# Performance work log

Measured on AMD Instinct MI355X. Metric: run time of the kernel, lower is better.

## Reference

```python
import jax, jax.numpy as jnp
import numpy as np

N_NODES = 100000
N_EDGES = 1600000
D_IN = 256
D_OUT = 128


def setup_inputs() -> dict:
    key = jax.random.key(0)
    k1, k2, k3, k4, k5, k6 = jax.random.split(key, 6)
    x = jax.random.normal(k1, (N_NODES, D_IN), dtype=jnp.float32)
    edge_src = jax.random.randint(k2, (N_EDGES,), 0, N_NODES, dtype=jnp.int32)
    edge_dst = jax.random.randint(k3, (N_EDGES,), 0, N_NODES, dtype=jnp.int32)
    edge_w = jax.random.uniform(k4, (N_EDGES,), dtype=jnp.float32)
    # GraphConvolution parameters (glorot-style scale)
    W = jax.random.normal(k5, (D_IN, D_OUT), dtype=jnp.float32) / np.sqrt(D_IN)
    b = jax.random.normal(k6, (D_OUT,), dtype=jnp.float32) * 0.01
    return {"x": x, "edge_src": edge_src, "edge_dst": edge_dst,
            "edge_w": edge_w, "W": W, "b": b}


def reference(x, edge_src, edge_dst, edge_w, W, b):
    # GraphConvolution: out = adj @ (x @ W) + b, adj given as weighted edge list
    support = x @ W                                   # [N, D_OUT] dense GEMM
    msgs = support[edge_src] * edge_w[:, None]        # [E, D_OUT] gather + scale
    out = jax.ops.segment_sum(msgs, edge_dst, num_segments=N_NODES)  # scatter-add
    return out + b
```

## Files before the change

kernel.cpp:

```cpp
#include <hip/hip_runtime.h>

#define N_NODES 100000
#define N_EDGES 1600000
#define D_IN 256
#define D_OUT 128

#define NPB 128
#define NB 782
#define REGION 2432
#define CHUNK 4096
#define NCHUNK 391
#define GEMM_BLOCKS 782

typedef __attribute__((ext_vector_type(8))) short bf16x8;
typedef __attribute__((ext_vector_type(4))) float f32x4;

__device__ __forceinline__ unsigned short f2bf(float f) {
    unsigned u = __float_as_uint(f);
    u += 0x7FFF + ((u >> 16) & 1);
    return (unsigned short)(u >> 16);
}
__device__ __forceinline__ float bflo(unsigned p) { return __uint_as_float(p << 16); }
__device__ __forceinline__ float bfhi(unsigned p) { return __uint_as_float(p & 0xFFFF0000u); }

__global__ void prep_kernel(const float* __restrict__ W,
                            unsigned short* __restrict__ Wt) {
    int idx = blockIdx.x * 256 + threadIdx.x;
    if (idx < D_OUT * D_IN) {
        int c = idx >> 8;
        int k = idx & 255;
        Wt[idx] = f2bf(W[(size_t)k * D_OUT + c]);
    }
}

union FusedSmem {
    int hist[NB];
    unsigned short wt[128 * 256];
};

__global__ __launch_bounds__(256) void fusedA_kernel(
        const float* __restrict__ x,
        const unsigned short* __restrict__ Wt,
        unsigned short* __restrict__ supb,
        const int* __restrict__ dst,
        int* __restrict__ counts) {
    __shared__ FusedSmem sm;
    int tid = threadIdx.x;

    if (blockIdx.x < NCHUNK) {
        int* hist = sm.hist;
        int e0 = blockIdx.x * CHUNK;
        for (int i = tid; i < NB; i += 256) hist[i] = 0;
        __syncthreads();
#pragma unroll
        for (int k = 0; k < 16; ++k) {
            int e = e0 + k * 256 + tid;
            if (e < N_EDGES) atomicAdd(&hist[dst[e] >> 7], 1);
        }
        __syncthreads();
        int* crow = counts + (size_t)blockIdx.x * NB;
        for (int i = tid; i < NB; i += 256) crow[i] = hist[i];
    } else {
        {
            const int4* wg = (const int4*)Wt;
            char* wl = (char*)sm.wt;
            for (int i = tid; i < 4096; i += 256) {
                int off = i * 16;
                int col = off >> 9;
                int soff = off ^ ((col & 7) << 4);
                *(int4*)(wl + soff) = wg[i];
            }
        }
        __syncthreads();

        int gb = blockIdx.x - NCHUNK;
        int w = tid >> 6;
        int lane = tid & 63;
        int r0 = (gb * 4 + w) * 32;
        int rowA0 = r0 + (lane & 15);
        int rowA1 = rowA0 + 16;
        int rowA0c = rowA0 < N_NODES ? rowA0 : N_NODES - 1;
        int rowA1c = rowA1 < N_NODES ? rowA1 : N_NODES - 1;
        int kgrp = (lane >> 4) * 8;

        f32x4 acc0[8], acc1[8];
#pragma unroll
        for (int t = 0; t < 8; ++t) {
            acc0[t] = (f32x4){0.f, 0.f, 0.f, 0.f};
            acc1[t] = (f32x4){0.f, 0.f, 0.f, 0.f};
        }

        const float* xr0 = x + (size_t)rowA0c * D_IN + kgrp;
        const float* xr1 = x + (size_t)rowA1c * D_IN + kgrp;
        int colbase = lane & 15;
        const char* wl = (const char*)sm.wt;

#pragma unroll
        for (int ks = 0; ks < 8; ++ks) {
            int k0 = ks * 32;
            float4 a0 = *(const float4*)(xr0 + k0);
            float4 a1 = *(const float4*)(xr0 + k0 + 4);
            float4 c0 = *(const float4*)(xr1 + k0);
            float4 c1 = *(const float4*)(xr1 + k0 + 4);
            bf16x8 af0, af1;
            af0[0] = (short)f2bf(a0.x); af0[1] = (short)f2bf(a0.y);
            af0[2] = (short)f2bf(a0.z); af0[3] = (short)f2bf(a0.w);
            af0[4] = (short)f2bf(a1.x); af0[5] = (short)f2bf(a1.y);
            af0[6] = (short)f2bf(a1.z); af0[7] = (short)f2bf(a1.w);
            af1[0] = (short)f2bf(c0.x); af1[1] = (short)f2bf(c0.y);
            af1[2] = (short)f2bf(c0.z); af1[3] = (short)f2bf(c0.w);
            af1[4] = (short)f2bf(c1.x); af1[5] = (short)f2bf(c1.y);
            af1[6] = (short)f2bf(c1.z); af1[7] = (short)f2bf(c1.w);
#pragma unroll
            for (int t = 0; t < 8; ++t) {
                int col = t * 16 + colbase;
                int boff = (col * 512 + (k0 + kgrp) * 2) ^ ((col & 7) << 4);
                bf16x8 bfrag = *(const bf16x8*)(wl + boff);
                acc0[t] = __builtin_amdgcn_mfma_f32_16x16x32_bf16(af0, bfrag,
                                                                  acc0[t], 0, 0, 0);
                acc1[t] = __builtin_amdgcn_mfma_f32_16x16x32_bf16(af1, bfrag,
                                                                  acc1[t], 0, 0, 0);
            }
        }

        __syncthreads();
        unsigned short* tl = sm.wt + (size_t)w * (16 * 136);
        int rgrp = (lane >> 4) * 4;
        int row = lane >> 2;
        int c4 = lane & 3;
#pragma unroll
        for (int tilei = 0; tilei < 2; ++tilei) {
            const f32x4* ac = tilei ? acc1 : acc0;
#pragma unroll
            for (int t = 0; t < 8; ++t)
#pragma unroll
                for (int j = 0; j < 4; ++j)
                    tl[(rgrp + j) * 136 + t * 16 + colbase] = f2bf(ac[t][j]);

            int orow = r0 + tilei * 16 + row;
            if (orow < N_NODES) {
#pragma unroll
                for (int u = 0; u < 4; ++u) {
                    int col0 = u * 32 + c4 * 8;
                    int4 v = *(const int4*)(tl + row * 136 + col0);
                    *(int4*)(supb + (size_t)orow * D_OUT + col0) = v;
                }
            }
        }
    }
}

__global__ __launch_bounds__(512) void scanB_kernel(
        const int* __restrict__ counts,
        int* __restrict__ starts,
        int* __restrict__ totals) {
    int wv = threadIdx.x >> 6, lane = threadIdx.x & 63;
    int bin = blockIdx.x * 8 + wv;
    if (bin >= NB) return;
    int carry = 0;
#pragma unroll
    for (int g = 0; g < 7; ++g) {
        int idx = g * 64 + lane;
        int v = (idx < NCHUNK) ? counts[(size_t)idx * NB + bin] : 0;
        int s = v;
#pragma unroll
        for (int d = 1; d < 64; d <<= 1) {
            int u = __shfl_up(s, d, 64);
            if (lane >= d) s += u;
        }
        if (idx < NCHUNK) starts[(size_t)idx * NB + bin] = carry + s - v;
        carry += __shfl(s, 63, 64);
    }
    if (lane == 0) totals[bin] = carry;
}

__global__ __launch_bounds__(512) void flushC_kernel(
        const int* __restrict__ src,
        const int* __restrict__ dst,
        const float* __restrict__ ew,
        const int* __restrict__ starts,
        int2* __restrict__ stg) {
    __shared__ int cur[NB];
    int tid = threadIdx.x;
    int e0 = blockIdx.x * CHUNK;

    const int* srow = starts + (size_t)blockIdx.x * NB;
    for (int i = tid; i < NB; i += 512) cur[i] = srow[i];
    __syncthreads();

#pragma unroll
    for (int k = 0; k < 8; ++k) {
        int e = e0 + k * 512 + tid;
        if (e < N_EDGES) {
            int d = dst[e];
            int bin = d >> 7;
            int pos = atomicAdd(&cur[bin], 1);
            if (pos < REGION)
                stg[(size_t)bin * REGION + pos] =
                    make_int2(src[e] | ((d & 127) << 17), __float_as_int(ew[e]));
        }
    }
}

__global__ __launch_bounds__(512) void sgather_kernel(
        const unsigned short* __restrict__ supb,
        const int2* __restrict__ stg,
        const int* __restrict__ totals,
        const float* __restrict__ b,
        float* __restrict__ out) {
    __shared__ int2 sorted[REGION];
    __shared__ int hist2[NPB];
    __shared__ int base2[NPB + 1];
    __shared__ int cur2[NPB];
    __shared__ int scanbuf[512];

    int tid = threadIdx.x;
    int bkt = blockIdx.x;
    int node0 = bkt * NPB;

    if (tid < NPB) hist2[tid] = 0;
    __syncthreads();

    int cnt = totals[bkt];
    if (cnt > REGION) cnt = REGION;
    const int2* sg = stg + (size_t)bkt * REGION;

    int2 tp[5];
    int dl[5];
#pragma unroll
    for (int k = 0; k < 5; ++k) {
        int e = tid + k * 512;
        dl[k] = -1;
        if (e < cnt) {
            tp[k] = sg[e];
            dl[k] = (tp[k].x >> 17) & 127;
            atomicAdd(&hist2[dl[k]], 1);
        }
    }
    __syncthreads();

    int v = (tid < NPB) ? hist2[tid] : 0;
    scanbuf[tid] = v;
    __syncthreads();
    for (int d = 1; d < NPB; d <<= 1) {
        int t = (tid >= d) ? scanbuf[tid - d] : 0;
        __syncthreads();
        scanbuf[tid] += t;
        __syncthreads();
    }
    if (tid < NPB) {
        base2[tid] = scanbuf[tid] - v;
        cur2[tid] = scanbuf[tid] - v;
    }
    if (tid == 0) base2[NPB] = cnt;
    __syncthreads();

#pragma unroll
    for (int k = 0; k < 5; ++k) {
        if (dl[k] >= 0) {
            int pos = atomicAdd(&cur2[dl[k]], 1);
            sorted[pos] = tp[k];
        }
    }
    __syncthreads();

    int wave = tid >> 6, lane = tid & 63;
    float2 bv = ((const float2*)b)[lane];

#pragma unroll 1
    for (int jj = 0; jj < 16; ++jj) {
        int j = wave * 16 + jj;
        int node = node0 + j;
        if (node >= N_NODES) break;
        int s = base2[j], t = base2[j + 1];
        float ax = 0.f, ay = 0.f;
        int e = s;
        for (; e + 3 < t; e += 4) {
            int2 t0 = sorted[e];
            int2 t1 = sorted[e + 1];
            int2 t2 = sorted[e + 2];
            int2 t3 = sorted[e + 3];
            unsigned p0 = *(const unsigned*)(supb + (size_t)(t0.x & 0x1FFFF) * D_OUT + 2 * lane);
            unsigned p1 = *(const unsigned*)(supb + (size_t)(t1.x & 0x1FFFF) * D_OUT + 2 * lane);
            unsigned p2 = *(const unsigned*)(supb + (size_t)(t2.x & 0x1FFFF) * D_OUT + 2 * lane);
            unsigned p3 = *(const unsigned*)(supb + (size_t)(t3.x & 0x1FFFF) * D_OUT + 2 * lane);
            float w0 = __int_as_float(t0.y);
            float w1 = __int_as_float(t1.y);
            float w2 = __int_as_float(t2.y);
            float w3 = __int_as_float(t3.y);
            ax += w0 * bflo(p0) + w1 * bflo(p1) + w2 * bflo(p2) + w3 * bflo(p3);
            ay += w0 * bfhi(p0) + w1 * bfhi(p1) + w2 * bfhi(p2) + w3 * bfhi(p3);
        }
        for (; e < t; ++e) {
            int2 t0 = sorted[e];
            unsigned p0 = *(const unsigned*)(supb + (size_t)(t0.x & 0x1FFFF) * D_OUT + 2 * lane);
            float w0 = __int_as_float(t0.y);
            ax += w0 * bflo(p0);
            ay += w0 * bfhi(p0);
        }
        ((float2*)(out + (size_t)node * D_OUT))[lane] =
            make_float2(ax + bv.x, ay + bv.y);
    }
}

extern "C" void kernel_launch(void* const* d_in, const int* in_sizes, int n_in,
                              void* d_out, int out_size, void* d_ws, size_t ws_size,
                              hipStream_t stream) {
    const float* x   = (const float*)d_in[0];
    const int* esrc  = (const int*)d_in[1];
    const int* edst  = (const int*)d_in[2];
    const float* ew  = (const float*)d_in[3];
    const float* W   = (const float*)d_in[4];
    const float* b   = (const float*)d_in[5];
    float* out = (float*)d_out;

    uint8_t* w8 = (uint8_t*)d_ws;
    unsigned short* supb = (unsigned short*)w8;
    int2* stg    = (int2*)(w8 + 25600000);
    int* counts  = (int*)(w8 + 40814592);
    int* starts  = (int*)(w8 + 42037640);
    int* totals  = (int*)(w8 + 43260688);
    unsigned short* Wt = (unsigned short*)(w8 + 43264000);

    prep_kernel<<<(D_OUT * D_IN + 255) / 256, 256, 0, stream>>>(W, Wt);

    fusedA_kernel<<<NCHUNK + GEMM_BLOCKS, 256, 0, stream>>>(
        x, Wt, supb, edst, counts);

    scanB_kernel<<<(NB + 7) / 8, 512, 0, stream>>>(counts, starts, totals);

    flushC_kernel<<<NCHUNK, 512, 0, stream>>>(esrc, edst, ew, starts, stg);

    sgather_kernel<<<NB, 512, 0, stream>>>(supb, stg, totals, b, out);
}
```

Before: 302.5 us.

## Restructure pipeline: fuse W prep into counting, fuse edge flush with GEMM

```diff
diff --git a/kernel.cpp b/kernel.cpp
--- a/kernel.cpp
+++ b/kernel.cpp
@@ -8,9 +8,10 @@
 #define NPB 128
 #define NB 782
 #define REGION 2432
-#define CHUNK 4096
-#define NCHUNK 391
-#define GEMM_BLOCKS 782
+#define CHUNK 16384
+#define NCHUNK 98
+#define PREP_BLOCKS 8
+#define GEMMB 391
 
 typedef __attribute__((ext_vector_type(8))) short bf16x8;
 typedef __attribute__((ext_vector_type(4))) float f32x4;
@@ -23,48 +24,100 @@
 __device__ __forceinline__ float bflo(unsigned p) { return __uint_as_float(p << 16); }
 __device__ __forceinline__ float bfhi(unsigned p) { return __uint_as_float(p & 0xFFFF0000u); }
 
-__global__ void prep_kernel(const float* __restrict__ W,
-                            unsigned short* __restrict__ Wt) {
-    int idx = blockIdx.x * 256 + threadIdx.x;
-    if (idx < D_OUT * D_IN) {
-        int c = idx >> 8;
-        int k = idx & 255;
-        Wt[idx] = f2bf(W[(size_t)k * D_OUT + c]);
-    }
-}
-
-union FusedSmem {
-    int hist[NB];
+__global__ __launch_bounds__(512) void countA_kernel(
+        const float* __restrict__ W,
+        unsigned short* __restrict__ Wt,
+        const int* __restrict__ dst,
+        int* __restrict__ counts) {
+    int tid = threadIdx.x;
+    if (blockIdx.x < NCHUNK) {
+        __shared__ int hist[NB];
+        int e0 = blockIdx.x * CHUNK;
+        for (int i = tid; i < NB; i += 512) hist[i] = 0;
+        __syncthreads();
+#pragma unroll
+        for (int k = 0; k < 32; ++k) {
+            int e = e0 + k * 512 + tid;
+            if (e < N_EDGES) atomicAdd(&hist[dst[e] >> 7], 1);
+        }
+        __syncthreads();
+        int* crow = counts + (size_t)blockIdx.x * NB;
+        for (int i = tid; i < NB; i += 512) crow[i] = hist[i];
+    } else {
+        int base = (int)(blockIdx.x - NCHUNK) * 4096;
+        for (int i = tid; i < 4096; i += 512) {
+            int idx = base + i;
+            int c = idx >> 8;
+            int k = idx & 255;
+            Wt[idx] = f2bf(W[(size_t)k * D_OUT + c]);
+        }
+    }
+}
+
+__global__ __launch_bounds__(512) void scanB_kernel(
+        const int* __restrict__ counts,
+        int* __restrict__ starts,
+        int* __restrict__ totals) {
+    int wv = threadIdx.x >> 6, lane = threadIdx.x & 63;
+    int bin = blockIdx.x * 8 + wv;
+    if (bin >= NB) return;
+    int carry = 0;
+#pragma unroll
+    for (int g = 0; g < 2; ++g) {
+        int idx = g * 64 + lane;
+        int v = (idx < NCHUNK) ? counts[(size_t)idx * NB + bin] : 0;
+        int s = v;
+#pragma unroll
+        for (int d = 1; d < 64; d <<= 1) {
+            int u = __shfl_up(s, d, 64);
+            if (lane >= d) s += u;
+        }
+        if (idx < NCHUNK) starts[(size_t)idx * NB + bin] = carry + s - v;
+        carry += __shfl(s, 63, 64);
+    }
+    if (lane == 0) totals[bin] = carry;
+}
+
+union Fused2Smem {
+    int cur[NB];
     unsigned short wt[128 * 256];
 };
 
-__global__ __launch_bounds__(256) void fusedA_kernel(
+__global__ __launch_bounds__(512) void fusedB_kernel(
         const float* __restrict__ x,
         const unsigned short* __restrict__ Wt,
         unsigned short* __restrict__ supb,
+        const int* __restrict__ src,
         const int* __restrict__ dst,
-        int* __restrict__ counts) {
-    __shared__ FusedSmem sm;
+        const float* __restrict__ ew,
+        const int* __restrict__ starts,
+        int2* __restrict__ stg) {
+    __shared__ Fused2Smem sm;
     int tid = threadIdx.x;
 
     if (blockIdx.x < NCHUNK) {
-        int* hist = sm.hist;
         int e0 = blockIdx.x * CHUNK;
-        for (int i = tid; i < NB; i += 256) hist[i] = 0;
-        __syncthreads();
-#pragma unroll
-        for (int k = 0; k < 16; ++k) {
-            int e = e0 + k * 256 + tid;
-            if (e < N_EDGES) atomicAdd(&hist[dst[e] >> 7], 1);
-        }
-        __syncthreads();
-        int* crow = counts + (size_t)blockIdx.x * NB;
-        for (int i = tid; i < NB; i += 256) crow[i] = hist[i];
+        const int* srow = starts + (size_t)blockIdx.x * NB;
+        for (int i = tid; i < NB; i += 512) sm.cur[i] = srow[i];
+        __syncthreads();
+#pragma unroll
+        for (int k = 0; k < 32; ++k) {
+            int e = e0 + k * 512 + tid;
+            if (e < N_EDGES) {
+                int d = dst[e];
+                int bin = d >> 7;
+                int pos = atomicAdd(&sm.cur[bin], 1);
+                if (pos < REGION)
+                    stg[(size_t)bin * REGION + pos] =
+                        make_int2(src[e] | ((d & 127) << 17),
+                                  __float_as_int(ew[e]));
+            }
+        }
     } else {
         {
             const int4* wg = (const int4*)Wt;
             char* wl = (char*)sm.wt;
-            for (int i = tid; i < 4096; i += 256) {
+            for (int i = tid; i < 4096; i += 512) {
                 int off = i * 16;
                 int col = off >> 9;
                 int soff = off ^ ((col & 7) << 4);
@@ -76,7 +129,7 @@
         int gb = blockIdx.x - NCHUNK;
         int w = tid >> 6;
         int lane = tid & 63;
-        int r0 = (gb * 4 + w) * 32;
+        int r0 = (gb * 8 + w) * 32;
         int rowA0 = r0 + (lane & 15);
         int rowA1 = rowA0 + 16;
         int rowA0c = rowA0 < N_NODES ? rowA0 : N_NODES - 1;
@@ -146,58 +199,6 @@
                     *(int4*)(supb + (size_t)orow * D_OUT + col0) = v;
                 }
             }
-        }
-    }
-}
-
-__global__ __launch_bounds__(512) void scanB_kernel(
-        const int* __restrict__ counts,
-        int* __restrict__ starts,
-        int* __restrict__ totals) {
-    int wv = threadIdx.x >> 6, lane = threadIdx.x & 63;
-    int bin = blockIdx.x * 8 + wv;
-    if (bin >= NB) return;
-    int carry = 0;
-#pragma unroll
-    for (int g = 0; g < 7; ++g) {
-        int idx = g * 64 + lane;
-        int v = (idx < NCHUNK) ? counts[(size_t)idx * NB + bin] : 0;
-        int s = v;
-#pragma unroll
-        for (int d = 1; d < 64; d <<= 1) {
-            int u = __shfl_up(s, d, 64);
-            if (lane >= d) s += u;
-        }
-        if (idx < NCHUNK) starts[(size_t)idx * NB + bin] = carry + s - v;
-        carry += __shfl(s, 63, 64);
-    }
-    if (lane == 0) totals[bin] = carry;
-}
-
-__global__ __launch_bounds__(512) void flushC_kernel(
-        const int* __restrict__ src,
-        const int* __restrict__ dst,
-        const float* __restrict__ ew,
-        const int* __restrict__ starts,
-        int2* __restrict__ stg) {
-    __shared__ int cur[NB];
-    int tid = threadIdx.x;
-    int e0 = blockIdx.x * CHUNK;
-
-    const int* srow = starts + (size_t)blockIdx.x * NB;
-    for (int i = tid; i < NB; i += 512) cur[i] = srow[i];
-    __syncthreads();
-
-#pragma unroll
-    for (int k = 0; k < 8; ++k) {
-        int e = e0 + k * 512 + tid;
-        if (e < N_EDGES) {
-            int d = dst[e];
-            int bin = d >> 7;
-            int pos = atomicAdd(&cur[bin], 1);
-            if (pos < REGION)
-                stg[(size_t)bin * REGION + pos] =
-                    make_int2(src[e] | ((d & 127) << 17), __float_as_int(ew[e]));
         }
     }
 }
@@ -318,18 +319,16 @@
     unsigned short* supb = (unsigned short*)w8;
     int2* stg    = (int2*)(w8 + 25600000);
     int* counts  = (int*)(w8 + 40814592);
-    int* starts  = (int*)(w8 + 42037640);
-    int* totals  = (int*)(w8 + 43260688);
-    unsigned short* Wt = (unsigned short*)(w8 + 43264000);
-
-    prep_kernel<<<(D_OUT * D_IN + 255) / 256, 256, 0, stream>>>(W, Wt);
-
-    fusedA_kernel<<<NCHUNK + GEMM_BLOCKS, 256, 0, stream>>>(
-        x, Wt, supb, edst, counts);
+    int* starts  = (int*)(w8 + 41121136);
+    int* totals  = (int*)(w8 + 41427680);
+    unsigned short* Wt = (unsigned short*)(w8 + 41430816);
+
+    countA_kernel<<<NCHUNK + PREP_BLOCKS, 512, 0, stream>>>(W, Wt, edst, counts);
 
     scanB_kernel<<<(NB + 7) / 8, 512, 0, stream>>>(counts, starts, totals);
 
-    flushC_kernel<<<NCHUNK, 512, 0, stream>>>(esrc, edst, ew, starts, stg);
+    fusedB_kernel<<<NCHUNK + GEMMB, 512, 0, stream>>>(
+        x, Wt, supb, esrc, edst, ew, starts, stg);
 
     sgather_kernel<<<NB, 512, 0, stream>>>(supb, stg, totals, b, out);
 }
```

Measured after the change: 309.8 us. 1.02x slower.
